# Kernel tuning notes

Measured on AMD Instinct MI355X. Metric: run time of the kernel, lower is better.

## Reference

```python
import jax, jax.numpy as jnp
import numpy as np

D_MODEL = 1024
N_HEAD = 16
D_K = 64
D_V = 64
D_INNER = 4096
MAX_REL = 16
EPS = 1e-6


def _rel_index(length_q, length_k):
    # Shaw-style clipped relative distance matrix -> indices into embedding table
    dist = jnp.arange(length_k)[None, :] - jnp.arange(length_q)[:, None]
    return jnp.clip(dist, -MAX_REL, MAX_REL) + MAX_REL  # [Lq, Lk] in [0, 2*MAX_REL]


def _layer_norm(x, gamma, beta):
    mu = jnp.mean(x, axis=-1, keepdims=True)
    var = jnp.var(x, axis=-1, keepdims=True)
    return (x - mu) / jnp.sqrt(var + EPS) * gamma + beta


def setup_inputs() -> dict:
    key = jax.random.key(0)
    ks = jax.random.split(key, 16)
    B, L = 8, 1024
    s = 0.02
    inp = {
        "q": jax.random.normal(ks[0], (B, L, D_MODEL), jnp.float32),
        "k": jax.random.normal(ks[1], (B, L, D_MODEL), jnp.float32),
        "v": jax.random.normal(ks[2], (B, L, D_MODEL), jnp.float32),
        "wq": jax.random.normal(ks[3], (D_MODEL, D_MODEL), jnp.float32) * s,
        "bq": jnp.zeros((D_MODEL,), jnp.float32),
        "wk": jax.random.normal(ks[4], (D_MODEL, D_MODEL), jnp.float32) * s,
        "bk": jnp.zeros((D_MODEL,), jnp.float32),
        "wv": jax.random.normal(ks[5], (D_MODEL, D_MODEL), jnp.float32) * s,
        "bv": jnp.zeros((D_MODEL,), jnp.float32),
        "wfc": jax.random.normal(ks[6], (D_MODEL, D_MODEL), jnp.float32) * s,
        "bfc": jnp.zeros((D_MODEL,), jnp.float32),
        "w1": jax.random.normal(ks[7], (D_MODEL, D_INNER), jnp.float32) * s,
        "b1": jnp.zeros((D_INNER,), jnp.float32),
        "w2": jax.random.normal(ks[8], (D_INNER, D_MODEL), jnp.float32) * s,
        "b2": jnp.zeros((D_MODEL,), jnp.float32),
        "ln_g": jnp.ones((D_MODEL,), jnp.float32),
        "ln_b": jnp.zeros((D_MODEL,), jnp.float32),
        "rel_k": jax.random.normal(ks[9], (2 * MAX_REL + 1, D_K), jnp.float32) * s,
        "rel_v": jax.random.normal(ks[10], (2 * MAX_REL + 1, D_V), jnp.float32) * s,
    }
    return inp


def reference(q, k, v, wq, bq, wk, bk, wv, bv, wfc, bfc, w1, b1, w2, b2, ln_g, ln_b, rel_k, rel_v):
    B, Lq, _ = q.shape
    Lk = k.shape[1]
    residual = q

    Q = q @ wq + bq  # [B, Lq, D]
    K = k @ wk + bk
    V = v @ wv + bv

    Qh = Q.reshape(B, Lq, N_HEAD, D_K)  # [B, Lq, H, dk]
    Kh = K.reshape(B, Lk, N_HEAD, D_K)
    Vh = V.reshape(B, Lk, N_HEAD, D_V)

    # content-content scores
    attn1 = jnp.einsum("bqhd,bkhd->bhqk", Qh, Kh)
    # content-position scores (Shaw relative position)
    idx = _rel_index(Lq, Lk)  # [Lq, Lk]
    k2 = rel_k[idx]           # [Lq, Lk, dk]
    attn2 = jnp.einsum("bqhd,qkd->bhqk", Qh, k2)

    attn = (attn1 + attn2) / jnp.sqrt(jnp.float32(D_K))
    attn = jax.nn.softmax(attn, axis=-1)  # dropout = identity (eval)

    weight1 = jnp.einsum("bhqk,bkhd->bhqd", attn, Vh)
    v2 = rel_v[idx]  # [Lq, Lk, dv]
    weight2 = jnp.einsum("bhqk,qkd->bhqd", attn, v2)

    out = (weight1 + weight2).transpose(0, 2, 1, 3).reshape(B, Lq, N_HEAD * D_V)
    out = out @ wfc + bfc
    out = out + residual
    out = _layer_norm(out, ln_g, ln_b)

    residual = out
    out2 = jax.nn.relu(out @ w1 + b1) @ w2 + b2
    out = _layer_norm(out2 + residual, ln_g, ln_b)  # same LN params reused, as in source
    return out
```

## Files before the change

kernel.cpp:

```cpp
#include <hip/hip_runtime.h>
#include <stdint.h>


typedef __bf16 bf16x8 __attribute__((ext_vector_type(8)));
typedef float  f32x4  __attribute__((ext_vector_type(4)));

__device__ __forceinline__ unsigned short f2bf(float f) {
  __bf16 h = (__bf16)f;
  union { __bf16 h; unsigned short u; } x; x.h = h;
  return x.u;
}
__device__ __forceinline__ float bf2f(unsigned short h) {
  union { unsigned u; float f; } x; x.u = ((unsigned)h) << 16; return x.f;
}

__device__ __forceinline__ void gload_lds16(
    const unsigned short* g,
    __attribute__((address_space(3))) unsigned int* l) {
  __builtin_amdgcn_global_load_lds(
      (const __attribute__((address_space(1))) unsigned int*)g, l, 16, 0, 0);
}

template<int EPI>
__global__ __launch_bounds__(256) void gemm_bt(
    const unsigned short* __restrict__ A,
    const unsigned short* __restrict__ Bt,
    const float* __restrict__ bias,
    void* __restrict__ Cout,
    int M, int N, int K)
{
  __shared__ __align__(16) unsigned short As[128 * 32];
  __shared__ __align__(16) unsigned short Bs[128 * 32];
  const int tid = threadIdx.x;
  const int lane = tid & 63, wv = tid >> 6;
  const int lq = lane >> 4, lm = lane & 15;
  const int wr = wv >> 1, wc = wv & 1;

  const int nx = gridDim.x;
  const int nwg = nx * gridDim.y;
  int bid = blockIdx.y * nx + blockIdx.x;
  bid = (bid & 7) * (nwg >> 3) + (bid >> 3);
  const int m0 = (bid / nx) * 128, n0 = (bid % nx) * 128;

  const unsigned short* ga0 = A  + (size_t)(m0 + (tid >> 2)) * K + (tid & 3) * 8;
  const unsigned short* gb0 = Bt + (size_t)(n0 + (tid >> 2)) * K + (tid & 3) * 8;
  const size_t rstep = (size_t)64 * K;

  __attribute__((address_space(3))) unsigned int* lA =
      (__attribute__((address_space(3))) unsigned int*)As + wv * 256;
  __attribute__((address_space(3))) unsigned int* lB =
      (__attribute__((address_space(3))) unsigned int*)Bs + wv * 256;

  const char* fa = (const char*)As + (wr * 64 + lm) * 64 + lq * 16;
  const char* fb = (const char*)Bs + (wc * 64 + lm) * 64 + lq * 16;

  f32x4 acc[4][4] = {};
  const int nk = K >> 5;
  for (int kt = 0; kt < nk; ++kt) {
    __syncthreads();
    gload_lds16(ga0,         lA);
    gload_lds16(ga0 + rstep, lA + 1024);
    gload_lds16(gb0,         lB);
    gload_lds16(gb0 + rstep, lB + 1024);
    ga0 += 32; gb0 += 32;
    __syncthreads();
    bf16x8 af[4], bfr[4];
    #pragma unroll
    for (int i = 0; i < 4; ++i) af[i]  = *(const bf16x8*)(fa + i * 16 * 64);
    #pragma unroll
    for (int j = 0; j < 4; ++j) bfr[j] = *(const bf16x8*)(fb + j * 16 * 64);
    #pragma unroll
    for (int i = 0; i < 4; ++i)
      #pragma unroll
      for (int j = 0; j < 4; ++j)
        acc[i][j] = __builtin_amdgcn_mfma_f32_16x16x32_bf16(af[i], bfr[j], acc[i][j], 0, 0, 0);
  }
  #pragma unroll
  for (int i = 0; i < 4; ++i) {
    #pragma unroll
    for (int j = 0; j < 4; ++j) {
      const int col = n0 + wc * 64 + j * 16 + lm;
      const float bv = bias[col];
      #pragma unroll
      for (int r = 0; r < 4; ++r) {
        const int row = m0 + wr * 64 + i * 16 + lq * 4 + r;
        float v = acc[i][j][r] + bv;
        if (EPI == 2) v = fmaxf(v, 0.0f);
        if (EPI == 1) ((float*)Cout)[(size_t)row * N + col] = v;
        else ((unsigned short*)Cout)[(size_t)row * N + col] = f2bf(v);
      }
    }
  }
}

__global__ __launch_bounds__(256) void tcast(
    const float* __restrict__ in, unsigned short* __restrict__ out, int R, int C)
{
  __shared__ float tile[32][33];
  const int tx = threadIdx.x & 31, ty = threadIdx.x >> 5;
  const int r0 = blockIdx.y * 32, c0 = blockIdx.x * 32;
  #pragma unroll
  for (int s = 0; s < 4; ++s)
    tile[ty + s * 8][tx] = in[(size_t)(r0 + ty + s * 8) * C + c0 + tx];
  __syncthreads();
  #pragma unroll
  for (int s = 0; s < 4; ++s)
    out[(size_t)(c0 + ty + s * 8) * R + r0 + tx] = f2bf(tile[tx][ty + s * 8]);
}

__global__ __launch_bounds__(256) void cast4(
    const float* __restrict__ in, unsigned short* __restrict__ out, int n)
{
  int i = (blockIdx.x * 256 + threadIdx.x) * 4;
  if (i < n) {
    float4 v = *(const float4*)(in + i);
    ushort4 o;
    o.x = f2bf(v.x); o.y = f2bf(v.y); o.z = f2bf(v.z); o.w = f2bf(v.w);
    *(ushort4*)(out + i) = o;
  }
}

__global__ __launch_bounds__(256) void vtrans(
    const unsigned short* __restrict__ VP, unsigned short* __restrict__ VPT)
{
  __shared__ unsigned short tile[64 * 66];
  const int pt = blockIdx.x, h = blockIdx.y, b = blockIdx.z;
  const int tid = threadIdx.x;
  const int p = tid >> 2, c0 = (tid & 3) * 16;
  const unsigned short* src = VP + (size_t)(b * 1024 + pt * 64 + p) * 1024 + h * 64 + c0;
  union { uint4 q; unsigned int u[4]; } t0, t1;
  t0.q = *(const uint4*)src;
  t1.q = *(const uint4*)(src + 8);
  #pragma unroll
  for (int e = 0; e < 4; ++e) {
    *(unsigned int*)&tile[p * 66 + c0 + e * 2]     = t0.u[e];
    *(unsigned int*)&tile[p * 66 + c0 + 8 + e * 2] = t1.u[e];
  }
  __syncthreads();
  const int d = tid >> 2, p0 = (tid & 3) * 16;
  union { uint4 q[2]; unsigned short s[16]; } ob;
  #pragma unroll
  for (int e = 0; e < 16; ++e) ob.s[e] = tile[(p0 + e) * 66 + d];
  unsigned short* dst = VPT + ((size_t)(h * 64 + d) * 8 + b) * 1024 + pt * 64 + p0;
  *(uint4*)dst       = ob.q[0];
  *(uint4*)(dst + 8) = ob.q[1];
}

__global__ __launch_bounds__(256, 3) void attn_flash(
    const unsigned short* __restrict__ Qp,
    const unsigned short* __restrict__ Kp,
    const unsigned short* __restrict__ VPT,
    const float* __restrict__ relk,
    const float* __restrict__ relv,
    unsigned short* __restrict__ ctx)
{
  int id = (blockIdx.z * gridDim.y + blockIdx.y) * gridDim.x + blockIdx.x;
  id = (id & 7) * 256 + (id >> 3);
  const int qt = id & 15, h = (id >> 4) & 15, b = id >> 8;

  const int tid = threadIdx.x;
  const int lane = tid & 63, wv = tid >> 6;
  const int lq = lane >> 4, lm = lane & 15;

  __shared__ __align__(16) unsigned short Kt[64][72];
  __shared__ __align__(16) unsigned short Vt[64][72];
  __shared__ __align__(16) unsigned short Pt[64][72];
  __shared__ __align__(16) unsigned short relvT[64][32];
  __shared__ float qrel_s[64][33];
  __shared__ float Racc[64][33];

  const float CE = 0.125f * 1.44269504088896340736f;

  const int tok0 = b * 1024 + qt * 64;

  for (int i = tid; i < 64 * 33; i += 256) {
    const int rr = i / 33, ss = i - rr * 33;
    Racc[rr][ss] = 0.0f;
  }
  for (int i = tid; i < 64 * 32; i += 256) {
    const int dd = i >> 5, ss = i & 31;
    relvT[dd][ss] = f2bf(relv[ss * 64 + dd]);
  }

  bf16x8 qf0, qf1;
  {
    const unsigned short* qg = Qp + (size_t)(tok0 + wv * 16 + lm) * 1024 + h * 64;
    qf0 = *(const bf16x8*)(qg + lq * 8);
    qf1 = *(const bf16x8*)(qg + 32 + lq * 8);
  }

  #pragma unroll
  for (int t = 0; t < 3; ++t) {
    const int bin = t * 16 + lm;
    union { bf16x8 v; unsigned short s[8]; } rk0, rk1;
    #pragma unroll
    for (int e = 0; e < 8; ++e) { rk0.s[e] = 0; rk1.s[e] = 0; }
    if (bin < 33) {
      const float* rp = relk + bin * 64 + lq * 8;
      #pragma unroll
      for (int e = 0; e < 8; ++e) {
        rk0.s[e] = f2bf(rp[e]);
        rk1.s[e] = f2bf(rp[32 + e]);
      }
    }
    f32x4 Sr = {};
    Sr = __builtin_amdgcn_mfma_f32_16x16x32_bf16(qf0, rk0.v, Sr, 0, 0, 0);
    Sr = __builtin_amdgcn_mfma_f32_16x16x32_bf16(qf1, rk1.v, Sr, 0, 0, 0);
    if (bin < 33) {
      #pragma unroll
      for (int r = 0; r < 4; ++r) qrel_s[wv * 16 + lq * 4 + r][bin] = Sr[r] * CE;
    }
  }
  __syncthreads();

  float q0a[4], q32a[4];
  #pragma unroll
  for (int r = 0; r < 4; ++r) {
    const int rowl = wv * 16 + lq * 4 + r;
    q0a[r]  = qrel_s[rowl][0];
    q32a[r] = qrel_s[rowl][32];
  }

  union { bf16x8 v; unsigned short s[8]; } one8;
  #pragma unroll
  for (int e = 0; e < 8; ++e) one8.s[e] = 0x3F80;

  f32x4 Oa[4] = {};
  f32x4 Rs = {};
  float r0a[4] = {0, 0, 0, 0}, r32a[4] = {0, 0, 0, 0};

  const int srow = tid >> 2, scol = (tid & 3) * 16;
  const unsigned short* kg = Kp + (size_t)(b * 1024 + srow) * 1024 + h * 64 + scol;
  const unsigned short* vg = VPT + ((size_t)(h * 64 + srow) * 8 + b) * 1024 + scol;
  const int qa0 = qt * 64 + wv * 16;

  const int pread = wv * 16 + ((lm & 3) << 2) + (lm >> 2);

  uint4 rk0_ = *(const uint4*)(kg);
  uint4 rk1_ = *(const uint4*)(kg + 8);
  uint4 rv0_ = *(const uint4*)(vg);
  uint4 rv1_ = *(const uint4*)(vg + 8);

  for (int kt = 0; kt < 16; ++kt) {
    __syncthreads();
    *(uint4*)&Kt[srow][scol]     = rk0_;
    *(uint4*)&Kt[srow][scol + 8] = rk1_;
    *(uint4*)&Vt[srow][scol]     = rv0_;
    *(uint4*)&Vt[srow][scol + 8] = rv1_;
    if (kt < 15) {
      kg += 64 * 1024;
      vg += 64;
      rk0_ = *(const uint4*)(kg);
      rk1_ = *(const uint4*)(kg + 8);
      rv0_ = *(const uint4*)(vg);
      rv1_ = *(const uint4*)(vg + 8);
    }
    __syncthreads();

    #pragma unroll
    for (int tj = 0; tj < 4; ++tj) {
      bf16x8 kf0 = *(const bf16x8*)(&Kt[tj * 16 + lm][lq * 8]);
      bf16x8 kf1 = *(const bf16x8*)(&Kt[tj * 16 + lm][32 + lq * 8]);
      f32x4 S = {};
      S = __builtin_amdgcn_mfma_f32_16x16x32_bf16(qf0, kf0, S, 0, 0, 0);
      S = __builtin_amdgcn_mfma_f32_16x16x32_bf16(qf1, kf1, S, 0, 0, 0);
      const int c0 = kt * 64 + tj * 16;
      const int prow0 = wv * 16 + lq;
      if (c0 + 31 <= qa0) {
        #pragma unroll
        for (int r = 0; r < 4; ++r) {
          const float p = __builtin_amdgcn_exp2f(fmaf(S[r], CE, q0a[r]));
          r0a[r] += p;
          Pt[prow0 + r * 4][tj * 16 + lm] = f2bf(p);
        }
      } else if (c0 >= qa0 + 31) {
        #pragma unroll
        for (int r = 0; r < 4; ++r) {
          const float p = __builtin_amdgcn_exp2f(fmaf(S[r], CE, q32a[r]));
          r32a[r] += p;
          Pt[prow0 + r * 4][tj * 16 + lm] = f2bf(p);
        }
      } else {
        const int kpos = c0 + lm;
        #pragma unroll
        for (int r = 0; r < 4; ++r) {
          const int rowl = wv * 16 + lq * 4 + r;
          const int dist = kpos - (qt * 64 + rowl);
          const int bin = (dist < -16 ? 0 : (dist > 16 ? 32 : dist + 16));
          const float p = __builtin_amdgcn_exp2f(fmaf(S[r], CE, qrel_s[rowl][bin]));
          if (bin == 0)       r0a[r]  += p;
          else if (bin == 32) r32a[r] += p;
          else Racc[rowl][bin] = p;
          Pt[prow0 + r * 4][tj * 16 + lm] = f2bf(p);
        }
      }
    }
    __syncthreads();
    bf16x8 pf0 = *(const bf16x8*)(&Pt[pread][lq * 8]);
    bf16x8 pf1 = *(const bf16x8*)(&Pt[pread][32 + lq * 8]);
    Rs = __builtin_amdgcn_mfma_f32_16x16x32_bf16(pf0, one8.v, Rs, 0, 0, 0);
    Rs = __builtin_amdgcn_mfma_f32_16x16x32_bf16(pf1, one8.v, Rs, 0, 0, 0);
    #pragma unroll
    for (int dt = 0; dt < 4; ++dt) {
      bf16x8 vf0 = *(const bf16x8*)(&Vt[dt * 16 + lm][lq * 8]);
      bf16x8 vf1 = *(const bf16x8*)(&Vt[dt * 16 + lm][32 + lq * 8]);
      Oa[dt] = __builtin_amdgcn_mfma_f32_16x16x32_bf16(pf0, vf0, Oa[dt], 0, 0, 0);
      Oa[dt] = __builtin_amdgcn_mfma_f32_16x16x32_bf16(pf1, vf1, Oa[dt], 0, 0, 0);
    }
  }

  #pragma unroll
  for (int r = 0; r < 4; ++r) {
    #pragma unroll
    for (int off = 1; off < 16; off <<= 1) {
      r0a[r]  += __shfl_xor(r0a[r],  off, 64);
      r32a[r] += __shfl_xor(r32a[r], off, 64);
    }
  }
  if (lm == 0) {
    #pragma unroll
    for (int r = 0; r < 4; ++r) Racc[wv * 16 + lq * 4 + r][0] = r0a[r];
  }
  __syncthreads();
  for (int i = tid; i < 64 * 32; i += 256) {
    const int rr = i >> 5, cc = i & 31;
    Pt[rr][cc] = f2bf(Racc[rr][cc]);
  }
  __syncthreads();

  bf16x8 raf = *(const bf16x8*)(&Pt[wv * 16 + lm][lq * 8]);
  #pragma unroll
  for (int dt = 0; dt < 4; ++dt) {
    bf16x8 rvb = *(const bf16x8*)(&relvT[dt * 16 + lm][lq * 8]);
    f32x4 O2 = {};
    O2 = __builtin_amdgcn_mfma_f32_16x16x32_bf16(raf, rvb, O2, 0, 0, 0);
    const float rv32 = relv[32 * 64 + dt * 16 + lm];
    #pragma unroll
    for (int r = 0; r < 4; ++r) {
      const int rowl = wv * 16 + lq * 4 + r;
      const float v = (Oa[dt][r] + O2[r] + r32a[r] * rv32) / Rs[r];
      ctx[(size_t)(tok0 + rowl) * 1024 + h * 64 + dt * 16 + lm] = f2bf(v);
    }
  }
}

template<bool WB>
__global__ __launch_bounds__(256) void ln_res(
    const float* __restrict__ x, const float* __restrict__ res,
    const float* __restrict__ g, const float* __restrict__ bta,
    float* __restrict__ of, unsigned short* __restrict__ ob)
{
  const int row = blockIdx.x;
  const int tid = threadIdx.x;
  __shared__ float red[8];
  const size_t base = (size_t)row * 1024 + tid * 4;
  const float4 xv = *(const float4*)(x + base);
  const float4 rv = *(const float4*)(res + base);
  float v0 = xv.x + rv.x, v1 = xv.y + rv.y, v2 = xv.z + rv.z, v3 = xv.w + rv.w;
  float s1 = v0 + v1 + v2 + v3;
  float s2 = v0 * v0 + v1 * v1 + v2 * v2 + v3 * v3;
  #pragma unroll
  for (int off = 1; off < 64; off <<= 1) {
    s1 += __shfl_xor(s1, off, 64);
    s2 += __shfl_xor(s2, off, 64);
  }
  const int wv = tid >> 6;
  if ((tid & 63) == 0) { red[wv * 2] = s1; red[wv * 2 + 1] = s2; }
  __syncthreads();
  s1 = red[0] + red[2] + red[4] + red[6];
  s2 = red[1] + red[3] + red[5] + red[7];
  const float mean = s1 * (1.f / 1024.f);
  const float var = s2 * (1.f / 1024.f) - mean * mean;
  const float rstd = rsqrtf(var + 1e-6f);
  const float4 gv = *(const float4*)(g + tid * 4);
  const float4 bv = *(const float4*)(bta + tid * 4);
  float y0 = (v0 - mean) * rstd * gv.x + bv.x;
  float y1 = (v1 - mean) * rstd * gv.y + bv.y;
  float y2 = (v2 - mean) * rstd * gv.z + bv.z;
  float y3 = (v3 - mean) * rstd * gv.w + bv.w;
  float4 yo; yo.x = y0; yo.y = y1; yo.z = y2; yo.w = y3;
  *(float4*)(of + base) = yo;
  if (WB) {
    ushort4 o;
    o.x = f2bf(y0); o.y = f2bf(y1); o.z = f2bf(y2); o.w = f2bf(y3);
    *(ushort4*)(ob + base) = o;
  }
}

extern "C" void kernel_launch(void* const* d_in, const int* in_sizes, int n_in,
                              void* d_out, int out_size, void* d_ws, size_t ws_size,
                              hipStream_t stream) {
  (void)in_sizes; (void)n_in; (void)out_size; (void)ws_size;
  const float* q    = (const float*)d_in[0];
  const float* k    = (const float*)d_in[1];
  const float* v    = (const float*)d_in[2];
  const float* wq   = (const float*)d_in[3];
  const float* bq   = (const float*)d_in[4];
  const float* wk   = (const float*)d_in[5];
  const float* bk   = (const float*)d_in[6];
  const float* wv_  = (const float*)d_in[7];
  const float* bv   = (const float*)d_in[8];
  const float* wfc  = (const float*)d_in[9];
  const float* bfc  = (const float*)d_in[10];
  const float* w1   = (const float*)d_in[11];
  const float* b1   = (const float*)d_in[12];
  const float* w2   = (const float*)d_in[13];
  const float* b2   = (const float*)d_in[14];
  const float* ln_g = (const float*)d_in[15];
  const float* ln_b = (const float*)d_in[16];
  const float* rel_k = (const float*)d_in[17];
  const float* rel_v = (const float*)d_in[18];

  char* ws = (char*)d_ws;
  const size_t MB = 1ull << 20;
  unsigned short* WQT  = (unsigned short*)(ws + 0 * MB);
  unsigned short* WKT  = (unsigned short*)(ws + 2 * MB);
  unsigned short* WVT  = (unsigned short*)(ws + 4 * MB);
  unsigned short* WFCT = (unsigned short*)(ws + 6 * MB);
  unsigned short* W1T  = (unsigned short*)(ws + 8 * MB);
  unsigned short* W2T  = (unsigned short*)(ws + 16 * MB);
  unsigned short* QP   = (unsigned short*)(ws + 24 * MB);
  unsigned short* KP   = (unsigned short*)(ws + 40 * MB);
  unsigned short* VP   = (unsigned short*)(ws + 56 * MB);
  unsigned short* QBF  = (unsigned short*)(ws + 72 * MB);
  unsigned short* KBF  = (unsigned short*)(ws + 88 * MB);
  unsigned short* VBF  = (unsigned short*)(ws + 104 * MB);
  unsigned short* VPT  = QBF;
  unsigned short* CTX  = KBF;
  float*          OTMP = (float*)(ws + 104 * MB);
  float*          X1F  = (float*)(ws + 24 * MB);
  unsigned short* X1BF = VP;
  unsigned short* HBUF = (unsigned short*)(ws + 72 * MB);
  float*          Y2   = (float*)(ws + 136 * MB);

  const dim3 blk(256);
  const int NTOK = 8192;

  tcast<<<dim3(32, 32), blk, 0, stream>>>(wq, WQT, 1024, 1024);
  tcast<<<dim3(32, 32), blk, 0, stream>>>(wk, WKT, 1024, 1024);
  tcast<<<dim3(32, 32), blk, 0, stream>>>(wv_, WVT, 1024, 1024);
  tcast<<<dim3(32, 32), blk, 0, stream>>>(wfc, WFCT, 1024, 1024);
  tcast<<<dim3(128, 32), blk, 0, stream>>>(w1, W1T, 1024, 4096);
  tcast<<<dim3(32, 128), blk, 0, stream>>>(w2, W2T, 4096, 1024);
  cast4<<<8192, blk, 0, stream>>>(q, QBF, NTOK * 1024);
  cast4<<<8192, blk, 0, stream>>>(k, KBF, NTOK * 1024);
  cast4<<<8192, blk, 0, stream>>>(v, VBF, NTOK * 1024);

  gemm_bt<0><<<dim3(8, 64), blk, 0, stream>>>(QBF, WQT, bq, QP, NTOK, 1024, 1024);
  gemm_bt<0><<<dim3(8, 64), blk, 0, stream>>>(KBF, WKT, bk, KP, NTOK, 1024, 1024);
  gemm_bt<0><<<dim3(8, 64), blk, 0, stream>>>(VBF, WVT, bv, VP, NTOK, 1024, 1024);

  vtrans<<<dim3(16, 16, 8), blk, 0, stream>>>(VP, VPT);

  attn_flash<<<dim3(16, 16, 8), blk, 0, stream>>>(QP, KP, VPT, rel_k, rel_v, CTX);

  gemm_bt<1><<<dim3(8, 64), blk, 0, stream>>>(CTX, WFCT, bfc, OTMP, NTOK, 1024, 1024);
  ln_res<true><<<8192, blk, 0, stream>>>(OTMP, q, ln_g, ln_b, X1F, X1BF);
  gemm_bt<2><<<dim3(32, 64), blk, 0, stream>>>(X1BF, W1T, b1, HBUF, NTOK, 4096, 1024);
  gemm_bt<1><<<dim3(8, 64), blk, 0, stream>>>(HBUF, W2T, b2, Y2, NTOK, 1024, 4096);
  ln_res<false><<<8192, blk, 0, stream>>>(Y2, X1F, ln_g, ln_b, (float*)d_out, nullptr);
}
```

Before: 647.2 us.

## Double-buffer GEMM LDS loads and batch QKV projections into one launch

The GEMM kernel now keeps two LDS buffers and issues global-to-LDS loads for the next K tile before computing on the current one. This removes one barrier per iteration and lets memory latency overlap with MFMA work. The three Q/K/V projection GEMMs are merged into a single launch using blockIdx.z with strided pointers, and launch bounds now request 4 blocks per CU. The merge depends on the workspace buffers sitting at the assumed fixed strides, and doubling LDS per block may limit occupancy.

```diff
diff --git a/kernel.cpp b/kernel.cpp
--- a/kernel.cpp
+++ b/kernel.cpp
@@ -22,19 +22,27 @@
 }
 
 template<int EPI>
-__global__ __launch_bounds__(256) void gemm_bt(
+__global__ __launch_bounds__(256, 4) void gemm_bt(
     const unsigned short* __restrict__ A,
     const unsigned short* __restrict__ Bt,
-    const float* __restrict__ bias,
+    const float* __restrict__ bias0,
+    const float* __restrict__ bias1,
+    const float* __restrict__ bias2,
     void* __restrict__ Cout,
-    int M, int N, int K)
-{
-  __shared__ __align__(16) unsigned short As[128 * 32];
-  __shared__ __align__(16) unsigned short Bs[128 * 32];
+    int M, int N, int K,
+    size_t sA, size_t sB, size_t sC)
+{
+  __shared__ __align__(16) unsigned short As[2][128 * 32];
+  __shared__ __align__(16) unsigned short Bs[2][128 * 32];
   const int tid = threadIdx.x;
   const int lane = tid & 63, wv = tid >> 6;
   const int lq = lane >> 4, lm = lane & 15;
   const int wr = wv >> 1, wc = wv & 1;
+
+  const int z = blockIdx.z;
+  const float* bias = (z == 0) ? bias0 : (z == 1) ? bias1 : bias2;
+  A  += (size_t)z * sA;
+  Bt += (size_t)z * sB;
 
   const int nx = gridDim.x;
   const int nwg = nx * gridDim.y;
@@ -55,26 +63,42 @@
   const char* fb = (const char*)Bs + (wc * 64 + lm) * 64 + lq * 16;
 
   f32x4 acc[4][4] = {};
-  const int nk = K >> 5;
-  for (int kt = 0; kt < nk; ++kt) {
-    __syncthreads();
-    gload_lds16(ga0,         lA);
-    gload_lds16(ga0 + rstep, lA + 1024);
-    gload_lds16(gb0,         lB);
-    gload_lds16(gb0 + rstep, lB + 1024);
-    ga0 += 32; gb0 += 32;
-    __syncthreads();
+
+  auto compute_tile = [&](int b) {
     bf16x8 af[4], bfr[4];
     #pragma unroll
-    for (int i = 0; i < 4; ++i) af[i]  = *(const bf16x8*)(fa + i * 16 * 64);
-    #pragma unroll
-    for (int j = 0; j < 4; ++j) bfr[j] = *(const bf16x8*)(fb + j * 16 * 64);
+    for (int i = 0; i < 4; ++i) af[i]  = *(const bf16x8*)(fa + b * 8192 + i * 1024);
+    #pragma unroll
+    for (int j = 0; j < 4; ++j) bfr[j] = *(const bf16x8*)(fb + b * 8192 + j * 1024);
     #pragma unroll
     for (int i = 0; i < 4; ++i)
       #pragma unroll
       for (int j = 0; j < 4; ++j)
         acc[i][j] = __builtin_amdgcn_mfma_f32_16x16x32_bf16(af[i], bfr[j], acc[i][j], 0, 0, 0);
-  }
+  };
+
+  const int nk = K >> 5;
+  gload_lds16(ga0,         lA);
+  gload_lds16(ga0 + rstep, lA + 1024);
+  gload_lds16(gb0,         lB);
+  gload_lds16(gb0 + rstep, lB + 1024);
+  ga0 += 32; gb0 += 32;
+  __syncthreads();
+
+  int cur = 0;
+  for (int kt = 0; kt < nk - 1; ++kt) {
+    const int nb = cur ^ 1;
+    gload_lds16(ga0,         lA + nb * 2048);
+    gload_lds16(ga0 + rstep, lA + nb * 2048 + 1024);
+    gload_lds16(gb0,         lB + nb * 2048);
+    gload_lds16(gb0 + rstep, lB + nb * 2048 + 1024);
+    ga0 += 32; gb0 += 32;
+    compute_tile(cur);
+    __syncthreads();
+    cur = nb;
+  }
+  compute_tile(cur);
+
   #pragma unroll
   for (int i = 0; i < 4; ++i) {
     #pragma unroll
@@ -87,7 +111,7 @@
         float v = acc[i][j][r] + bv;
         if (EPI == 2) v = fmaxf(v, 0.0f);
         if (EPI == 1) ((float*)Cout)[(size_t)row * N + col] = v;
-        else ((unsigned short*)Cout)[(size_t)row * N + col] = f2bf(v);
+        else ((unsigned short*)Cout + (size_t)z * sC)[(size_t)row * N + col] = f2bf(v);
       }
     }
   }
@@ -446,17 +470,20 @@
   cast4<<<8192, blk, 0, stream>>>(k, KBF, NTOK * 1024);
   cast4<<<8192, blk, 0, stream>>>(v, VBF, NTOK * 1024);
 
-  gemm_bt<0><<<dim3(8, 64), blk, 0, stream>>>(QBF, WQT, bq, QP, NTOK, 1024, 1024);
-  gemm_bt<0><<<dim3(8, 64), blk, 0, stream>>>(KBF, WKT, bk, KP, NTOK, 1024, 1024);
-  gemm_bt<0><<<dim3(8, 64), blk, 0, stream>>>(VBF, WVT, bv, VP, NTOK, 1024, 1024);
+  gemm_bt<0><<<dim3(8, 64, 3), blk, 0, stream>>>(
+      QBF, WQT, bq, bk, bv, QP, NTOK, 1024, 1024,
+      (size_t)8 * MB, (size_t)1 * MB, (size_t)8 * MB);
 
   vtrans<<<dim3(16, 16, 8), blk, 0, stream>>>(VP, VPT);
 
   attn_flash<<<dim3(16, 16, 8), blk, 0, stream>>>(QP, KP, VPT, rel_k, rel_v, CTX);
 
-  gemm_bt<1><<<dim3(8, 64), blk, 0, stream>>>(CTX, WFCT, bfc, OTMP, NTOK, 1024, 1024);
+  gemm_bt<1><<<dim3(8, 64), blk, 0, stream>>>(CTX, WFCT, bfc, bfc, bfc, OTMP,
+                                              NTOK, 1024, 1024, 0, 0, 0);
   ln_res<true><<<8192, blk, 0, stream>>>(OTMP, q, ln_g, ln_b, X1F, X1BF);
-  gemm_bt<2><<<dim3(32, 64), blk, 0, stream>>>(X1BF, W1T, b1, HBUF, NTOK, 4096, 1024);
-  gemm_bt<1><<<dim3(8, 64), blk, 0, stream>>>(HBUF, W2T, b2, Y2, NTOK, 1024, 4096);
+  gemm_bt<2><<<dim3(32, 64), blk, 0, stream>>>(X1BF, W1T, b1, b1, b1, HBUF,
+                                               NTOK, 4096, 1024, 0, 0, 0);
+  gemm_bt<1><<<dim3(8, 64), blk, 0, stream>>>(HBUF, W2T, b2, b2, b2, Y2,
+                                              NTOK, 1024, 4096, 0, 0, 0);
   ln_res<false><<<8192, blk, 0, stream>>>(Y2, X1F, ln_g, ln_b, (float*)d_out, nullptr);
 }
```

New measurement: 610.9 us. 5.6% less time.
